# Optimization experiments

Hardware: AMD Instinct MI355X
Metric: run time of the kernel (lower is better)

Reference implementation:

```python
import jax, jax.numpy as jnp
import numpy as np

N_NODES = 100000
NFEAT, NHID, NCLASS = 128, 64, 40
N_EDGES = 1600000


def setup_inputs() -> dict:
    key = jax.random.key(0)
    k1, k2, k3, k4, k5, k6 = jax.random.split(key, 6)
    x = jax.random.normal(k1, (N_NODES, NFEAT), dtype=jnp.float32)
    edge_index = jax.random.randint(k2, (2, N_EDGES), 0, N_NODES, dtype=jnp.int64)
    s1 = 1.0 / np.sqrt(NFEAT)
    s2 = 1.0 / np.sqrt(NHID)
    W1 = jax.random.uniform(k3, (NFEAT, NHID), jnp.float32, -s1, s1)
    b1 = jax.random.uniform(k4, (NHID,), jnp.float32, -s1, s1)
    W2 = jax.random.uniform(k5, (NHID, NCLASS), jnp.float32, -s2, s2)
    b2 = jax.random.uniform(k6, (NCLASS,), jnp.float32, -s2, s2)
    return {"x": x, "edge_index": edge_index, "W1": W1, "b1": b1, "W2": W2, "b2": b2}


def _gcn_conv(x, W, b, src, dst, n_nodes):
    # linear
    h = x @ W + b  # [N, out]
    # degree of source nodes (self-loops already included in src/dst)
    deg = jax.ops.segment_sum(jnp.ones_like(src, dtype=h.dtype), src, num_segments=n_nodes)
    dinv = deg ** -0.5  # deg >= 1 due to self-loops
    norm = dinv[src] * dinv[dst]  # [E]
    msg = norm[:, None] * h[src]  # gather + normalize, [E, out]
    return jax.ops.segment_sum(msg, dst, num_segments=n_nodes)  # scatter-add


def reference(x, edge_index, W1, b1, W2, b2):
    n = x.shape[0]
    loop = jnp.arange(n, dtype=edge_index.dtype)
    src = jnp.concatenate([edge_index[0], loop])
    dst = jnp.concatenate([edge_index[1], loop])
    h = _gcn_conv(x, W1, b1, src, dst, n)
    h = jax.nn.relu(h)
    # dropout is identity in eval mode
    h = _gcn_conv(h, W2, b2, src, dst, n)
    return jax.nn.log_softmax(h, axis=1)
```

## Files before the change

kernel.cpp:

```cpp
#include <hip/hip_runtime.h>
#include <math.h>

#define NFEAT 128
#define NHID 64
#define NCLASS 40
#define NCHUNK 64
#define RANGE_H 32768
#define RANGE_S 16384

typedef _Float16 half4_t __attribute__((ext_vector_type(4)));
typedef _Float16 half8_t __attribute__((ext_vector_type(8)));
typedef float f32x4 __attribute__((ext_vector_type(4)));

__global__ __launch_bounds__(1024) void histdeg_kernel(
    const int* __restrict__ src, const int* __restrict__ dst, int E, int n,
    int nrange, unsigned short* __restrict__ deg_p,
    unsigned short* __restrict__ hist_p) {
    __shared__ unsigned int degc[RANGE_H / 2];
    __shared__ unsigned int histc[RANGE_H / 2];
    int c = blockIdx.x / nrange;
    int r = blockIdx.x - c * nrange;
    int r0 = r * RANGE_H;
    for (int i = threadIdx.x; i < RANGE_H / 2; i += 1024) {
        degc[i] = 0u;
        histc[i] = 0u;
    }
    __syncthreads();
    int e0 = (int)((long long)E * c / NCHUNK);
    int e1 = (int)((long long)E * (c + 1) / NCHUNK);
    for (int e = e0 + threadIdx.x * 4; e + 4 <= e1; e += 4096) {
        int4 s4 = *(const int4*)(src + e);
        int4 d4 = *(const int4*)(dst + e);
        int ss[4] = {s4.x, s4.y, s4.z, s4.w};
        int dd[4] = {d4.x, d4.y, d4.z, d4.w};
#pragma unroll
        for (int k = 0; k < 4; ++k) {
            int s = ss[k] - r0, d = dd[k] - r0;
            if ((unsigned)s < (unsigned)RANGE_H)
                atomicAdd(&degc[s >> 1], 1u << ((s & 1) * 16));
            if ((unsigned)d < (unsigned)RANGE_H)
                atomicAdd(&histc[d >> 1], 1u << ((d & 1) * 16));
        }
    }
    int tb = e0 + ((e1 - e0) & ~3);
    for (int e = tb + threadIdx.x; e < e1; e += 1024) {
        int s = src[e] - r0, d = dst[e] - r0;
        if ((unsigned)s < (unsigned)RANGE_H)
            atomicAdd(&degc[s >> 1], 1u << ((s & 1) * 16));
        if ((unsigned)d < (unsigned)RANGE_H)
            atomicAdd(&histc[d >> 1], 1u << ((d & 1) * 16));
    }
    __syncthreads();
    int hi = n - r0; if (hi > RANGE_H) hi = RANGE_H;
    for (int i = threadIdx.x; i < hi; i += 1024) {
        unsigned dv = (degc[i >> 1] >> ((i & 1) * 16)) & 0xFFFFu;
        unsigned hv = (histc[i >> 1] >> ((i & 1) * 16)) & 0xFFFFu;
        deg_p[(size_t)c * n + r0 + i] = (unsigned short)dv;
        hist_p[(size_t)c * n + r0 + i] = (unsigned short)hv;
    }
}

__global__ void reduce_kernel(const unsigned short* __restrict__ deg_p,
                              const unsigned short* __restrict__ hist_p,
                              float* __restrict__ dinv,
                              int* __restrict__ htot, int n) {
    int i = blockIdx.x * blockDim.x + threadIdx.x;
    if (i >= n) return;
    int d = 1, h = 0;
#pragma unroll 8
    for (int c = 0; c < NCHUNK; ++c) {
        d += deg_p[(size_t)c * n + i];
        h += hist_p[(size_t)c * n + i];
    }
    dinv[i] = rsqrtf((float)d);
    htot[i] = h;
}

__global__ void scan_block_kernel(const int* __restrict__ hist,
                                  int* __restrict__ scanned,
                                  int* __restrict__ bsums, int n) {
    __shared__ int tmp[256];
    int i = blockIdx.x * 256 + threadIdx.x;
    int v = (i < n) ? hist[i] : 0;
    tmp[threadIdx.x] = v;
    __syncthreads();
#pragma unroll
    for (int off = 1; off < 256; off <<= 1) {
        int t = (threadIdx.x >= off) ? tmp[threadIdx.x - off] : 0;
        __syncthreads();
        tmp[threadIdx.x] += t;
        __syncthreads();
    }
    if (i < n) scanned[i] = tmp[threadIdx.x] - v;
    if (threadIdx.x == 255) bsums[blockIdx.x] = tmp[255];
}

__global__ void scan_partials_kernel(int* __restrict__ bsums, int nb) {
    __shared__ int tmp[512];
    int v = (threadIdx.x < nb) ? bsums[threadIdx.x] : 0;
    tmp[threadIdx.x] = v;
    __syncthreads();
#pragma unroll
    for (int off = 1; off < 512; off <<= 1) {
        int t = (threadIdx.x >= off) ? tmp[threadIdx.x - off] : 0;
        __syncthreads();
        tmp[threadIdx.x] += t;
        __syncthreads();
    }
    if (threadIdx.x < nb) bsums[threadIdx.x] = tmp[threadIdx.x] - v;
}

__global__ void scan_add_kernel(const int* __restrict__ scanned,
                                const int* __restrict__ bsums,
                                int* __restrict__ row_start, int n, int E) {
    int i = blockIdx.x * 256 + threadIdx.x;
    if (i < n) row_start[i] = scanned[i] + bsums[blockIdx.x];
    if (i == 0) row_start[n] = E;
}

__global__ void base_kernel(const int* __restrict__ row_start,
                            const unsigned short* __restrict__ hist_p,
                            int* __restrict__ bases, int n) {
    int i = blockIdx.x * blockDim.x + threadIdx.x;
    if (i >= n) return;
    int r = row_start[i];
#pragma unroll 8
    for (int c = 0; c < NCHUNK; ++c) {
        bases[(size_t)c * n + i] = r;
        r += hist_p[(size_t)c * n + i];
    }
}

__global__ __launch_bounds__(1024) void scatter_kernel(
    const int* __restrict__ src, const int* __restrict__ dst, int E, int n,
    int nrange, const int* __restrict__ bases, int* __restrict__ es) {
    __shared__ int cur[RANGE_S];
    int c = blockIdx.x / nrange;
    int r = blockIdx.x - c * nrange;
    int r0 = r * RANGE_S;
    int hi = n - r0; if (hi > RANGE_S) hi = RANGE_S;
    for (int i = threadIdx.x; i < hi; i += 1024)
        cur[i] = bases[(size_t)c * n + r0 + i];
    __syncthreads();
    int e0 = (int)((long long)E * c / NCHUNK);
    int e1 = (int)((long long)E * (c + 1) / NCHUNK);
    for (int e = e0 + threadIdx.x * 4; e + 4 <= e1; e += 4096) {
        int4 s4 = *(const int4*)(src + e);
        int4 d4 = *(const int4*)(dst + e);
        int ss[4] = {s4.x, s4.y, s4.z, s4.w};
        int dd[4] = {d4.x, d4.y, d4.z, d4.w};
#pragma unroll
        for (int k = 0; k < 4; ++k) {
            int d = dd[k] - r0;
            if ((unsigned)d < (unsigned)hi) {
                int pos = atomicAdd(&cur[d], 1);
                es[pos] = ss[k];
            }
        }
    }
    int tb = e0 + ((e1 - e0) & ~3);
    for (int e = tb + threadIdx.x; e < e1; e += 1024) {
        int d = dst[e] - r0;
        if ((unsigned)d < (unsigned)hi) {
            int pos = atomicAdd(&cur[d], 1);
            es[pos] = src[e];
        }
    }
}

__global__ __launch_bounds__(256) void gemm1_mfma_kernel(
    const float* __restrict__ x, const float* __restrict__ W1,
    const float* __restrict__ b1, const float* __restrict__ dinv,
    _Float16* __restrict__ H1, int n) {
    int wave = threadIdx.x >> 6;
    int lane = threadIdx.x & 63;
    int lr = lane & 15;
    int kg = lane >> 4;
    half8_t bf[4][4];
    float b1v[4];
#pragma unroll
    for (int t = 0; t < 4; ++t) {
        int col = t * 16 + lr;
        b1v[t] = b1[col];
#pragma unroll
        for (int ks = 0; ks < 4; ++ks) {
            int kb = ks * 32 + kg * 8;
            half8_t hb;
#pragma unroll
            for (int j = 0; j < 8; ++j) hb[j] = (_Float16)W1[(kb + j) * NHID + col];
            bf[ks][t] = hb;
        }
    }
    int nt16 = (n + 15) >> 4;
    for (int gt = blockIdx.x * 4 + wave; gt < nt16; gt += gridDim.x * 4) {
        int m0 = gt * 16;
        int arow = m0 + lr; if (arow >= n) arow = n - 1;
        f32x4 acc[4] = {f32x4{0,0,0,0}, f32x4{0,0,0,0}, f32x4{0,0,0,0}, f32x4{0,0,0,0}};
#pragma unroll
        for (int ks = 0; ks < 4; ++ks) {
            const float* ap = x + (size_t)arow * NFEAT + ks * 32 + kg * 8;
            float4 a0 = *(const float4*)ap;
            float4 a1 = *(const float4*)(ap + 4);
            half8_t af;
            af[0] = (_Float16)a0.x; af[1] = (_Float16)a0.y;
            af[2] = (_Float16)a0.z; af[3] = (_Float16)a0.w;
            af[4] = (_Float16)a1.x; af[5] = (_Float16)a1.y;
            af[6] = (_Float16)a1.z; af[7] = (_Float16)a1.w;
#pragma unroll
            for (int t = 0; t < 4; ++t)
                acc[t] = __builtin_amdgcn_mfma_f32_16x16x32_f16(af, bf[ks][t], acc[t], 0, 0, 0);
        }
        int r0 = m0 + kg * 4;
        float dv[4];
#pragma unroll
        for (int r = 0; r < 4; ++r) {
            int rr = r0 + r;
            dv[r] = (rr < n) ? dinv[rr] : 0.f;
        }
#pragma unroll
        for (int t = 0; t < 4; ++t)
#pragma unroll
            for (int r = 0; r < 4; ++r) {
                int rr = r0 + r;
                if (rr < n)
                    H1[(size_t)rr * NHID + t * 16 + lr] =
                        (_Float16)((acc[t][r] + b1v[t]) * dv[r]);
            }
    }
}

__global__ __launch_bounds__(256) void agg1_kernel(
    const int* __restrict__ es, const int* __restrict__ row_start,
    const float* __restrict__ dinv, const _Float16* __restrict__ H1,
    _Float16* __restrict__ AGG, int n) {
    int wave = threadIdx.x >> 6;
    int lane = threadIdx.x & 63;
    int q = lane >> 4;
    int m = lane & 15;
    int stride = gridDim.x * 4;
    for (int node = blockIdx.x * 4 + wave; node < n; node += stride) {
        int e0 = row_start[node], e1 = row_start[node + 1];
        float a0 = 0.f, a1 = 0.f, a2 = 0.f, a3 = 0.f;
        for (int e = e0; e < e1; e += 64) {
            int cnt = e1 - e; if (cnt > 64) cnt = 64;
            int myE = es[e + ((lane < cnt) ? lane : 0)];
            for (int j = 0; j < cnt; j += 16) {
#pragma unroll
                for (int p = 0; p < 4; ++p) {
                    int jj = j + 4 * p + q;
                    int rr = __shfl(myE, jj, 64);
                    if (jj < cnt) {
                        int off = (rr << 6) + (m << 2);
                        half4_t v = *(const half4_t*)(H1 + off);
                        a0 += (float)v[0]; a1 += (float)v[1];
                        a2 += (float)v[2]; a3 += (float)v[3];
                    }
                }
            }
        }
        if (q == 0) {
            half4_t v = *(const half4_t*)(H1 + (node << 6) + (m << 2));
            a0 += (float)v[0]; a1 += (float)v[1];
            a2 += (float)v[2]; a3 += (float)v[3];
        }
        a0 += __shfl_xor(a0, 16, 64); a0 += __shfl_xor(a0, 32, 64);
        a1 += __shfl_xor(a1, 16, 64); a1 += __shfl_xor(a1, 32, 64);
        a2 += __shfl_xor(a2, 16, 64); a2 += __shfl_xor(a2, 32, 64);
        a3 += __shfl_xor(a3, 16, 64); a3 += __shfl_xor(a3, 32, 64);
        float di = dinv[node];
        if (lane < 16) {
            half4_t o;
            o[0] = (_Float16)fmaxf(a0 * di, 0.f);
            o[1] = (_Float16)fmaxf(a1 * di, 0.f);
            o[2] = (_Float16)fmaxf(a2 * di, 0.f);
            o[3] = (_Float16)fmaxf(a3 * di, 0.f);
            *(half4_t*)(AGG + (node << 6) + (lane << 2)) = o;
        }
    }
}

__global__ __launch_bounds__(256) void gemm2_mfma_kernel(
    const _Float16* __restrict__ AGG, const float* __restrict__ W2,
    const float* __restrict__ b2, const float* __restrict__ dinv,
    _Float16* __restrict__ H2, int n) {
    int wave = threadIdx.x >> 6;
    int lane = threadIdx.x & 63;
    int lr = lane & 15;
    int kg = lane >> 4;
    half8_t bf[2][3];
    float b2v[3];
#pragma unroll
    for (int t = 0; t < 3; ++t) {
        int col = t * 16 + lr;
        b2v[t] = (col < NCLASS) ? b2[col] : 0.f;
#pragma unroll
        for (int ks = 0; ks < 2; ++ks) {
            int kb = ks * 32 + kg * 8;
            half8_t hb;
#pragma unroll
            for (int j = 0; j < 8; ++j)
                hb[j] = (col < NCLASS) ? (_Float16)W2[(kb + j) * NCLASS + col]
                                       : (_Float16)0.f;
            bf[ks][t] = hb;
        }
    }
    int nt16 = (n + 15) >> 4;
    for (int gt = blockIdx.x * 4 + wave; gt < nt16; gt += gridDim.x * 4) {
        int m0 = gt * 16;
        int arow = m0 + lr; if (arow >= n) arow = n - 1;
        f32x4 acc[3] = {f32x4{0,0,0,0}, f32x4{0,0,0,0}, f32x4{0,0,0,0}};
#pragma unroll
        for (int ks = 0; ks < 2; ++ks) {
            half8_t af = *(const half8_t*)(AGG + ((size_t)arow << 6) + ks * 32 + kg * 8);
#pragma unroll
            for (int t = 0; t < 3; ++t)
                acc[t] = __builtin_amdgcn_mfma_f32_16x16x32_f16(af, bf[ks][t], acc[t], 0, 0, 0);
        }
        int r0 = m0 + kg * 4;
        float dv[4];
#pragma unroll
        for (int r = 0; r < 4; ++r) {
            int rr = r0 + r;
            dv[r] = (rr < n) ? dinv[rr] : 0.f;
        }
#pragma unroll
        for (int t = 0; t < 3; ++t) {
            int col = t * 16 + lr;
            if (col < NCLASS) {
#pragma unroll
                for (int r = 0; r < 4; ++r) {
                    int rr = r0 + r;
                    if (rr < n)
                        H2[(size_t)rr * NCLASS + col] =
                            (_Float16)((acc[t][r] + b2v[t]) * dv[r]);
                }
            }
        }
    }
}

__global__ __launch_bounds__(256) void agg2_lsm_kernel(
    const int* __restrict__ es, const int* __restrict__ row_start,
    const float* __restrict__ dinv, const _Float16* __restrict__ H2,
    float* __restrict__ out, int n) {
    int wave = threadIdx.x >> 6;
    int lane = threadIdx.x & 63;
    int q = lane >> 4;
    int m = lane & 15;
    bool valid = (m < 10);
    int stride = gridDim.x * 4;
    for (int node = blockIdx.x * 4 + wave; node < n; node += stride) {
        int e0 = row_start[node], e1 = row_start[node + 1];
        float a0 = 0.f, a1 = 0.f, a2 = 0.f, a3 = 0.f;
        for (int e = e0; e < e1; e += 64) {
            int cnt = e1 - e; if (cnt > 64) cnt = 64;
            int myE = es[e + ((lane < cnt) ? lane : 0)];
            for (int j = 0; j < cnt; j += 16) {
#pragma unroll
                for (int p = 0; p < 4; ++p) {
                    int jj = j + 4 * p + q;
                    int rr = __shfl(myE, jj, 64);
                    if (valid && jj < cnt) {
                        int off = (((rr << 2) + rr) << 3) + (m << 2);
                        half4_t v = *(const half4_t*)(H2 + off);
                        a0 += (float)v[0]; a1 += (float)v[1];
                        a2 += (float)v[2]; a3 += (float)v[3];
                    }
                }
            }
        }
        if (q == 0 && valid) {
            int off = (((node << 2) + node) << 3) + (m << 2);
            half4_t v = *(const half4_t*)(H2 + off);
            a0 += (float)v[0]; a1 += (float)v[1];
            a2 += (float)v[2]; a3 += (float)v[3];
        }
        a0 += __shfl_xor(a0, 16, 64); a0 += __shfl_xor(a0, 32, 64);
        a1 += __shfl_xor(a1, 16, 64); a1 += __shfl_xor(a1, 32, 64);
        a2 += __shfl_xor(a2, 16, 64); a2 += __shfl_xor(a2, 32, 64);
        a3 += __shfl_xor(a3, 16, 64); a3 += __shfl_xor(a3, 32, 64);
        float di = dinv[node];
        float v0 = a0 * di, v1 = a1 * di, v2 = a2 * di, v3 = a3 * di;
        float vmax = valid ? fmaxf(fmaxf(v0, v1), fmaxf(v2, v3)) : -INFINITY;
#pragma unroll
        for (int off = 8; off; off >>= 1) vmax = fmaxf(vmax, __shfl_xor(vmax, off, 64));
        float sume = valid ? (__expf(v0 - vmax) + __expf(v1 - vmax) +
                              __expf(v2 - vmax) + __expf(v3 - vmax)) : 0.f;
#pragma unroll
        for (int off = 8; off; off >>= 1) sume += __shfl_xor(sume, off, 64);
        float lse = __logf(sume) + vmax;
        if (lane < 10) {
            float4 o = make_float4(v0 - lse, v1 - lse, v2 - lse, v3 - lse);
            *(float4*)(out + (size_t)node * NCLASS + 4 * lane) = o;
        }
    }
}

extern "C" void kernel_launch(void* const* d_in, const int* in_sizes, int n_in,
                              void* d_out, int out_size, void* d_ws, size_t ws_size,
                              hipStream_t stream) {
    const float* x  = (const float*)d_in[0];
    const int*   ei = (const int*)d_in[1];
    const float* W1 = (const float*)d_in[2];
    const float* b1 = (const float*)d_in[3];
    const float* W2 = (const float*)d_in[4];
    const float* b2 = (const float*)d_in[5];
    float* out = (float*)d_out;

    const int n = in_sizes[0] / NFEAT;
    const int E = in_sizes[1] / 2;
    const int* src = ei;
    const int* dst = ei + E;
    const int nrange_h = (n + RANGE_H - 1) / RANGE_H;
    const int nrange_s = (n + RANGE_S - 1) / RANGE_S;

    char* ws = (char*)d_ws;
    float*          dinv      = (float*)(ws + 0);
    int*            htot      = (int*)(ws + (512 << 10));
    int*            scanned   = (int*)(ws + (1024 << 10));
    int*            row_start = (int*)(ws + (1536 << 10));
    int*            bsums     = (int*)(ws + (2048 << 10));
    unsigned short* deg_p     = (unsigned short*)(ws + (3u << 20));
    unsigned short* hist_p    = (unsigned short*)(ws + (16u << 20));
    int*            bases     = (int*)(ws + (29u << 20));
    int*            es        = (int*)(ws + (3u << 20));
    _Float16*       H2        = (_Float16*)(ws + (16u << 20));
    _Float16*       H1        = (_Float16*)(ws + (29u << 20));
    _Float16*       AGG       = (_Float16*)(ws + (42u << 20));

    const int blk = 256;
    const int nblk_n = (n + blk - 1) / blk;

    histdeg_kernel<<<NCHUNK * nrange_h, 1024, 0, stream>>>(src, dst, E, n, nrange_h,
                                                           deg_p, hist_p);
    reduce_kernel<<<nblk_n, blk, 0, stream>>>(deg_p, hist_p, dinv, htot, n);

    scan_block_kernel<<<nblk_n, blk, 0, stream>>>(htot, scanned, bsums, n);
    scan_partials_kernel<<<1, 512, 0, stream>>>(bsums, nblk_n);
    scan_add_kernel<<<nblk_n, blk, 0, stream>>>(scanned, bsums, row_start, n, E);
    base_kernel<<<nblk_n, blk, 0, stream>>>(row_start, hist_p, bases, n);

    scatter_kernel<<<NCHUNK * nrange_s, 1024, 0, stream>>>(src, dst, E, n, nrange_s,
                                                           bases, es);

    gemm1_mfma_kernel<<<512, blk, 0, stream>>>(x, W1, b1, dinv, H1, n);

    agg1_kernel<<<4096, blk, 0, stream>>>(es, row_start, dinv, H1, AGG, n);

    gemm2_mfma_kernel<<<512, blk, 0, stream>>>(AGG, W2, b2, dinv, H2, n);

    agg2_lsm_kernel<<<4096, blk, 0, stream>>>(es, row_start, dinv, H2, out, n);
}
```

Baseline: 306.4 us.

## Store H1 as FP8 e4m3, split H2 into aligned planes, accumulate agg2 in fp16

The layer-1 hidden features are now quantized to FP8 e4m3 instead of fp16, which halves the bytes gathered per edge in the first aggregation. H2 is split into a 32-column plane and an 8-column plane so each row gather is power-of-two aligned. The second aggregation accumulates and reduces in packed fp16 rather than fp32. Together these cut gather bandwidth and ALU work, at the cost of noticeably lower precision and a risk of exceeding the accuracy tolerance.

```diff
diff --git a/kernel.cpp b/kernel.cpp
--- a/kernel.cpp
+++ b/kernel.cpp
@@ -1,4 +1,5 @@
 #include <hip/hip_runtime.h>
+#include <hip/hip_fp8.h>
 #include <math.h>
 
 #define NFEAT 128
@@ -11,6 +12,12 @@
 typedef _Float16 half4_t __attribute__((ext_vector_type(4)));
 typedef _Float16 half8_t __attribute__((ext_vector_type(8)));
 typedef float f32x4 __attribute__((ext_vector_type(4)));
+
+__device__ __forceinline__ float fp8f(unsigned b) {
+    __hip_fp8_e4m3 h;
+    h.__x = (__hip_fp8_storage_t)b;
+    return (float)h;
+}
 
 __global__ __launch_bounds__(1024) void histdeg_kernel(
     const int* __restrict__ src, const int* __restrict__ dst, int E, int n,
@@ -171,7 +178,7 @@
 __global__ __launch_bounds__(256) void gemm1_mfma_kernel(
     const float* __restrict__ x, const float* __restrict__ W1,
     const float* __restrict__ b1, const float* __restrict__ dinv,
-    _Float16* __restrict__ H1, int n) {
+    unsigned char* __restrict__ H1f8, int n) {
     int wave = threadIdx.x >> 6;
     int lane = threadIdx.x & 63;
     int lr = lane & 15;
@@ -222,16 +229,17 @@
 #pragma unroll
             for (int r = 0; r < 4; ++r) {
                 int rr = r0 + r;
-                if (rr < n)
-                    H1[(size_t)rr * NHID + t * 16 + lr] =
-                        (_Float16)((acc[t][r] + b1v[t]) * dv[r]);
+                if (rr < n) {
+                    __hip_fp8_e4m3 q((acc[t][r] + b1v[t]) * dv[r]);
+                    H1f8[((size_t)rr << 6) + t * 16 + lr] = (unsigned char)q.__x;
+                }
             }
     }
 }
 
 __global__ __launch_bounds__(256) void agg1_kernel(
     const int* __restrict__ es, const int* __restrict__ row_start,
-    const float* __restrict__ dinv, const _Float16* __restrict__ H1,
+    const float* __restrict__ dinv, const unsigned char* __restrict__ H1f8,
     _Float16* __restrict__ AGG, int n) {
     int wave = threadIdx.x >> 6;
     int lane = threadIdx.x & 63;
@@ -250,18 +258,21 @@
                     int jj = j + 4 * p + q;
                     int rr = __shfl(myE, jj, 64);
                     if (jj < cnt) {
-                        int off = (rr << 6) + (m << 2);
-                        half4_t v = *(const half4_t*)(H1 + off);
-                        a0 += (float)v[0]; a1 += (float)v[1];
-                        a2 += (float)v[2]; a3 += (float)v[3];
+                        unsigned w = *(const unsigned*)(H1f8 + ((size_t)rr << 6) + (m << 2));
+                        a0 += fp8f(w & 0xFFu);
+                        a1 += fp8f((w >> 8) & 0xFFu);
+                        a2 += fp8f((w >> 16) & 0xFFu);
+                        a3 += fp8f(w >> 24);
                     }
                 }
             }
         }
         if (q == 0) {
-            half4_t v = *(const half4_t*)(H1 + (node << 6) + (m << 2));
-            a0 += (float)v[0]; a1 += (float)v[1];
-            a2 += (float)v[2]; a3 += (float)v[3];
+            unsigned w = *(const unsigned*)(H1f8 + ((size_t)node << 6) + (m << 2));
+            a0 += fp8f(w & 0xFFu);
+            a1 += fp8f((w >> 8) & 0xFFu);
+            a2 += fp8f((w >> 16) & 0xFFu);
+            a3 += fp8f(w >> 24);
         }
         a0 += __shfl_xor(a0, 16, 64); a0 += __shfl_xor(a0, 32, 64);
         a1 += __shfl_xor(a1, 16, 64); a1 += __shfl_xor(a1, 32, 64);
@@ -274,7 +285,7 @@
             o[1] = (_Float16)fmaxf(a1 * di, 0.f);
             o[2] = (_Float16)fmaxf(a2 * di, 0.f);
             o[3] = (_Float16)fmaxf(a3 * di, 0.f);
-            *(half4_t*)(AGG + (node << 6) + (lane << 2)) = o;
+            *(half4_t*)(AGG + ((size_t)node << 6) + (lane << 2)) = o;
         }
     }
 }
@@ -282,7 +293,7 @@
 __global__ __launch_bounds__(256) void gemm2_mfma_kernel(
     const _Float16* __restrict__ AGG, const float* __restrict__ W2,
     const float* __restrict__ b2, const float* __restrict__ dinv,
-    _Float16* __restrict__ H2, int n) {
+    _Float16* __restrict__ H2a, _Float16* __restrict__ H2b, int n) {
     int wave = threadIdx.x >> 6;
     int lane = threadIdx.x & 63;
     int lr = lane & 15;
@@ -326,13 +337,15 @@
 #pragma unroll
         for (int t = 0; t < 3; ++t) {
             int col = t * 16 + lr;
-            if (col < NCLASS) {
-#pragma unroll
-                for (int r = 0; r < 4; ++r) {
-                    int rr = r0 + r;
-                    if (rr < n)
-                        H2[(size_t)rr * NCLASS + col] =
-                            (_Float16)((acc[t][r] + b2v[t]) * dv[r]);
+#pragma unroll
+            for (int r = 0; r < 4; ++r) {
+                int rr = r0 + r;
+                if (rr < n) {
+                    _Float16 val = (_Float16)((acc[t][r] + b2v[t]) * dv[r]);
+                    if (col < 32)
+                        H2a[((size_t)rr << 5) + col] = val;
+                    else if (col < NCLASS)
+                        H2b[((size_t)rr << 3) + (col - 32)] = val;
                 }
             }
         }
@@ -341,8 +354,8 @@
 
 __global__ __launch_bounds__(256) void agg2_lsm_kernel(
     const int* __restrict__ es, const int* __restrict__ row_start,
-    const float* __restrict__ dinv, const _Float16* __restrict__ H2,
-    float* __restrict__ out, int n) {
+    const float* __restrict__ dinv, const _Float16* __restrict__ H2a,
+    const _Float16* __restrict__ H2b, float* __restrict__ out, int n) {
     int wave = threadIdx.x >> 6;
     int lane = threadIdx.x & 63;
     int q = lane >> 4;
@@ -351,7 +364,7 @@
     int stride = gridDim.x * 4;
     for (int node = blockIdx.x * 4 + wave; node < n; node += stride) {
         int e0 = row_start[node], e1 = row_start[node + 1];
-        float a0 = 0.f, a1 = 0.f, a2 = 0.f, a3 = 0.f;
+        half4_t acc4 = {(_Float16)0, (_Float16)0, (_Float16)0, (_Float16)0};
         for (int e = e0; e < e1; e += 64) {
             int cnt = e1 - e; if (cnt > 64) cnt = 64;
             int myE = es[e + ((lane < cnt) ? lane : 0)];
@@ -361,26 +374,31 @@
                     int jj = j + 4 * p + q;
                     int rr = __shfl(myE, jj, 64);
                     if (valid && jj < cnt) {
-                        int off = (((rr << 2) + rr) << 3) + (m << 2);
-                        half4_t v = *(const half4_t*)(H2 + off);
-                        a0 += (float)v[0]; a1 += (float)v[1];
-                        a2 += (float)v[2]; a3 += (float)v[3];
+                        const _Float16* ptr = (m < 8)
+                            ? H2a + (((size_t)rr << 5) + (m << 2))
+                            : H2b + (((size_t)rr << 3) + ((m & 7) << 2));
+                        acc4 += *(const half4_t*)ptr;
                     }
                 }
             }
         }
         if (q == 0 && valid) {
-            int off = (((node << 2) + node) << 3) + (m << 2);
-            half4_t v = *(const half4_t*)(H2 + off);
-            a0 += (float)v[0]; a1 += (float)v[1];
-            a2 += (float)v[2]; a3 += (float)v[3];
-        }
-        a0 += __shfl_xor(a0, 16, 64); a0 += __shfl_xor(a0, 32, 64);
-        a1 += __shfl_xor(a1, 16, 64); a1 += __shfl_xor(a1, 32, 64);
-        a2 += __shfl_xor(a2, 16, 64); a2 += __shfl_xor(a2, 32, 64);
-        a3 += __shfl_xor(a3, 16, 64); a3 += __shfl_xor(a3, 32, 64);
+            const _Float16* ptr = (m < 8)
+                ? H2a + (((size_t)node << 5) + (m << 2))
+                : H2b + (((size_t)node << 3) + ((m & 7) << 2));
+            acc4 += *(const half4_t*)ptr;
+        }
+        union { half4_t h; int i[2]; } u, w;
+        u.h = acc4;
+        w.i[0] = __shfl_xor(u.i[0], 16, 64);
+        w.i[1] = __shfl_xor(u.i[1], 16, 64);
+        u.h += w.h;
+        w.i[0] = __shfl_xor(u.i[0], 32, 64);
+        w.i[1] = __shfl_xor(u.i[1], 32, 64);
+        u.h += w.h;
         float di = dinv[node];
-        float v0 = a0 * di, v1 = a1 * di, v2 = a2 * di, v3 = a3 * di;
+        float v0 = (float)u.h[0] * di, v1 = (float)u.h[1] * di;
+        float v2 = (float)u.h[2] * di, v3 = (float)u.h[3] * di;
         float vmax = valid ? fmaxf(fmaxf(v0, v1), fmaxf(v2, v3)) : -INFINITY;
 #pragma unroll
         for (int off = 8; off; off >>= 1) vmax = fmaxf(vmax, __shfl_xor(vmax, off, 64));
@@ -424,9 +442,10 @@
     unsigned short* hist_p    = (unsigned short*)(ws + (16u << 20));
     int*            bases     = (int*)(ws + (29u << 20));
     int*            es        = (int*)(ws + (3u << 20));
-    _Float16*       H2        = (_Float16*)(ws + (16u << 20));
-    _Float16*       H1        = (_Float16*)(ws + (29u << 20));
-    _Float16*       AGG       = (_Float16*)(ws + (42u << 20));
+    unsigned char*  H1f8      = (unsigned char*)(ws + (16u << 20));
+    _Float16*       H2a       = (_Float16*)(ws + (23u << 20));
+    _Float16*       H2b      = (_Float16*)(ws + (30u << 20));
+    _Float16*       AGG       = (_Float16*)(ws + (32u << 20));
 
     const int blk = 256;
     const int nblk_n = (n + blk - 1) / blk;
@@ -443,11 +462,11 @@
     scatter_kernel<<<NCHUNK * nrange_s, 1024, 0, stream>>>(src, dst, E, n, nrange_s,
                                                            bases, es);
 
-    gemm1_mfma_kernel<<<512, blk, 0, stream>>>(x, W1, b1, dinv, H1, n);
-
-    agg1_kernel<<<4096, blk, 0, stream>>>(es, row_start, dinv, H1, AGG, n);
-
-    gemm2_mfma_kernel<<<512, blk, 0, stream>>>(AGG, W2, b2, dinv, H2, n);
-
-    agg2_lsm_kernel<<<4096, blk, 0, stream>>>(es, row_start, dinv, H2, out, n);
-}
+    gemm1_mfma_kernel<<<512, blk, 0, stream>>>(x, W1, b1, dinv, H1f8, n);
+
+    agg1_kernel<<<4096, blk, 0, stream>>>(es, row_start, dinv, H1f8, AGG, n);
+
+    gemm2_mfma_kernel<<<512, blk, 0, stream>>>(AGG, W2, b2, dinv, H2a, H2b, n);
+
+    agg2_lsm_kernel<<<4096, blk, 0, stream>>>(es, row_start, dinv, H2a, H2b, out, n);
+}
```

Result: no change. 302.4 us (-1.3%).
